# Kernel tuning notes

Hardware: AMD Instinct MI355X
Metric: run time of the kernel (lower is better)

## Reference

```python
import jax, jax.numpy as jnp
import numpy as np

B, T, S = 1, 8, 1024
HID, H = 1152, 16
D = HID // H  # 72
EPS = 1e-6


def rmsnorm(t, gamma):
    # t: [b,t,s,h,d], gamma: [h,d] per-head learnable scale (QKNorm)
    var = jnp.mean(jnp.square(t), axis=-1, keepdims=True)
    return t * jax.lax.rsqrt(var + EPS) * gamma


def setup_inputs() -> dict:
    key = jax.random.key(0)
    ks = jax.random.split(key, 8)
    sc = lambda fan_in: 1.0 / np.sqrt(fan_in)
    x = jax.random.normal(ks[0], (B, T, S, HID), dtype=jnp.float32)
    Wq = jax.random.normal(ks[1], (HID, HID), dtype=jnp.float32) * sc(HID)
    bq = jnp.zeros((HID,), dtype=jnp.float32)
    Wkv = jax.random.normal(ks[2], (HID, 2 * HID), dtype=jnp.float32) * sc(HID)
    bkv = jnp.zeros((2 * HID,), dtype=jnp.float32)
    q_gamma = jnp.ones((H, D), dtype=jnp.float32)
    k_gamma = jnp.ones((H, D), dtype=jnp.float32)
    Wo = jax.random.normal(ks[3], (HID, HID), dtype=jnp.float32) * sc(HID)
    return {"x": x, "Wq": Wq, "bq": bq, "Wkv": Wkv, "bkv": bkv,
            "q_gamma": q_gamma, "k_gamma": k_gamma, "Wo": Wo}


def reference(x, Wq, bq, Wkv, bkv, q_gamma, k_gamma, Wo):
    b, t, s, _ = x.shape
    q = (x @ Wq + bq).reshape(b, t, s, H, D)
    kv = x @ Wkv + bkv
    k, v = jnp.split(kv, 2, axis=-1)
    k = k.reshape(b, t, s, H, D)
    v = v.reshape(b, t, s, H, D)
    q = rmsnorm(q, q_gamma)
    k = rmsnorm(k, k_gamma)
    # NOTE: original applies no 1/sqrt(d) scaling (QKNorm replaces it)
    attn_weight = jnp.einsum('btqhd,btkhd->bthqk', q, k)
    attn = jax.nn.softmax(attn_weight, axis=-1)
    out = jnp.einsum('bthqk,btkhd->btqhd', attn, v).reshape(b, t, s, HID)
    return out @ Wo
```

## Files before the change

kernel.cpp:

```cpp
#include <hip/hip_runtime.h>


typedef __attribute__((ext_vector_type(4))) short s16x4;
typedef __attribute__((ext_vector_type(8))) short s16x8;
typedef __attribute__((ext_vector_type(4))) float f32x4;
typedef __attribute__((ext_vector_type(16))) float f32x16;

__device__ __forceinline__ unsigned short f2b(float x) {
  unsigned u = __float_as_uint(x);
  u += 0x7FFFu + ((u >> 16) & 1u);
  return (unsigned short)(u >> 16);
}
__device__ __forceinline__ float b2f(unsigned short u) {
  return __uint_as_float(((unsigned)u) << 16);
}
__device__ __forceinline__ void gld16(const void* g, void* l) {
  __builtin_amdgcn_global_load_lds(
      (const __attribute__((address_space(1))) void*)g,
      (__attribute__((address_space(3))) void*)l, 16, 0, 0);
}

__global__ __launch_bounds__(256) void cvt_bf16_kernel(const float* __restrict__ in,
                                                       unsigned short* __restrict__ out,
                                                       int n16) {
  int i = blockIdx.x * 256 + threadIdx.x;
  if (i >= n16) return;
  const float4* p = (const float4*)(in + (size_t)i * 16);
  float4 a = p[0], b = p[1], c = p[2], d = p[3];
  s16x8 r0, r1;
  r0[0] = (short)f2b(a.x); r0[1] = (short)f2b(a.y); r0[2] = (short)f2b(a.z); r0[3] = (short)f2b(a.w);
  r0[4] = (short)f2b(c.x); r0[5] = (short)f2b(c.y); r0[6] = (short)f2b(c.z); r0[7] = (short)f2b(c.w);
  r1[0] = (short)f2b(b.x); r1[1] = (short)f2b(b.y); r1[2] = (short)f2b(b.z); r1[3] = (short)f2b(b.w);
  r1[4] = (short)f2b(d.x); r1[5] = (short)f2b(d.y); r1[6] = (short)f2b(d.z); r1[7] = (short)f2b(d.w);
  *(s16x8*)(out + (size_t)i * 16) = r0;
  *(s16x8*)(out + (size_t)i * 16 + 8) = r1;
}

__global__ __launch_bounds__(256) void transpose_cvt_kernel(const float* __restrict__ W,
                                                            unsigned short* __restrict__ WT,
                                                            int K, int N) {
  __shared__ float tile[32][33];
  int n0 = blockIdx.x * 32, k0 = blockIdx.y * 32;
  int tx = threadIdx.x, ty = threadIdx.y;
#pragma unroll
  for (int i = 0; i < 4; i++)
    tile[ty + i * 8][tx] = W[(size_t)(k0 + ty + i * 8) * N + n0 + tx];
  __syncthreads();
  int stx = (tx & 19) | ((tx & 4) << 1) | ((tx & 8) >> 1);
#pragma unroll
  for (int i = 0; i < 4; i++)
    WT[(size_t)(n0 + ty + i * 8) * K + k0 + stx] = f2b(tile[tx][ty + i * 8]);
}

template <int MODE>
__global__ __launch_bounds__(256) void gemm_bt_kernel(const unsigned short* __restrict__ A,
                                                      const unsigned short* __restrict__ BT,
                                                      const float* __restrict__ biasq,
                                                      const float* __restrict__ biaskv,
                                                      int N, int gx,
                                                      float* __restrict__ outF,
                                                      unsigned short* __restrict__ qn,
                                                      unsigned short* __restrict__ kn,
                                                      unsigned short* __restrict__ vt) {
  constexpr int K = 1152;
  constexpr int NT = K / 32;
  __shared__ __align__(16) unsigned short As[3 * 4096];
  __shared__ __align__(16) unsigned short Bs[3 * 4096];
  int tid = threadIdx.x;
  int lane = tid & 63, wave = tid >> 6;
  int wr = (wave >> 1) * 64, wc = (wave & 1) * 64;
  int l31 = lane & 31, lh = lane >> 5;
  int bid = blockIdx.x;
  int xcd = bid & 7;
  int w = bid >> 3;
  int st = w / 24, inner = w - st * 24;
  int ibx = inner % 3, iby = inner / 3;
  int bx = st * 3 + ibx;
  int by = xcd * 8 + iby;
  int brow = by * 128, bcol = bx * 128;
  const unsigned short* AsrcP[2];
  const unsigned short* BsrcP[2];
  int dst0[2];
#pragma unroll
  for (int i = 0; i < 2; i++) {
    int c = tid + 256 * i;
    int row = c >> 2, j = c & 3;
    int ch = j ^ ((row >> 1) & 3);
    AsrcP[i] = A + (size_t)(brow + row) * K + ch * 8;
    BsrcP[i] = BT + (size_t)(bcol + row) * K + ch * 8;
    dst0[i] = (wave * 64 + 256 * i) * 8;
  }
#define STAGE(KT, BUF)                                          \
  {                                                             \
    int kb = (KT) * 32;                                         \
    gld16(AsrcP[0] + kb, &As[(BUF) * 4096 + dst0[0]]);          \
    gld16(BsrcP[0] + kb, &Bs[(BUF) * 4096 + dst0[0]]);          \
    gld16(AsrcP[1] + kb, &As[(BUF) * 4096 + dst0[1]]);          \
    gld16(BsrcP[1] + kb, &Bs[(BUF) * 4096 + dst0[1]]);          \
  }
  int fr = (l31 >> 1) & 3;
  int slotk[2] = {(lh ^ fr) * 8, ((2 + lh) ^ fr) * 8};
  STAGE(0, 0);
  STAGE(1, 1);
  f32x16 acc[2][2] = {};
  int cur = 0;
  for (int kt = 0; kt < NT; kt++) {
    if (kt < NT - 1)
      asm volatile("s_waitcnt vmcnt(4)\n\ts_barrier" ::: "memory");
    else
      asm volatile("s_waitcnt vmcnt(0)\n\ts_barrier" ::: "memory");
    if (kt + 2 < NT) {
      int nb = (cur == 0) ? 2 : cur - 1;
      STAGE(kt + 2, nb);
    }
    int ab = cur * 4096;
#pragma unroll
    for (int kk = 0; kk < 2; kk++) {
      int so = slotk[kk];
      s16x8 af[2], bf[2];
#pragma unroll
      for (int m = 0; m < 2; m++)
        af[m] = *(const s16x8*)&As[ab + (wr + m * 32 + l31) * 32 + so];
#pragma unroll
      for (int n = 0; n < 2; n++)
        bf[n] = *(const s16x8*)&Bs[ab + (wc + n * 32 + l31) * 32 + so];
      __builtin_amdgcn_s_setprio(1);
#pragma unroll
      for (int m = 0; m < 2; m++)
#pragma unroll
        for (int n = 0; n < 2; n++)
          acc[m][n] = __builtin_amdgcn_mfma_f32_32x32x16_bf16(af[m], bf[n], acc[m][n], 0, 0, 0);
      __builtin_amdgcn_s_setprio(0);
    }
    cur = (cur == 2) ? 0 : cur + 1;
  }
#undef STAGE
#pragma unroll
  for (int m = 0; m < 2; m++) {
#pragma unroll
    for (int n = 0; n < 2; n++) {
#pragma unroll
      for (int reg = 0; reg < 16; reg++) {
        int grow = brow + wr + m * 32 + (reg & 3) + 8 * (reg >> 2) + 4 * lh;
        int gcol = bcol + wc + n * 32 + l31;
        float v = acc[m][n][reg];
        if (MODE == 0) {
          outF[(size_t)grow * N + gcol] = v;
        } else {
          v += (gcol < 1152) ? biasq[gcol] : biaskv[gcol - 1152];
          int t = grow >> 10, s = grow & 1023;
          if (gcol < 2304) {
            int c = (gcol < 1152) ? gcol : gcol - 1152;
            int h = c / 72, d = c - h * 72;
            unsigned short* dst = (gcol < 1152) ? qn : kn;
            dst[((size_t)((t * 16 + h) * 1024 + s)) * 96 + d] = f2b(v);
          } else {
            int c = gcol - 2304;
            int h = c / 72, d = c - h * 72;
            vt[((size_t)((t * 16 + h) * 80 + d)) * 1024 + s] = f2b(v);
          }
        }
      }
    }
  }
}

__global__ __launch_bounds__(256) void rmsnorm2_kernel(unsigned short* __restrict__ qn,
                                                       unsigned short* __restrict__ kn,
                                                       const float* __restrict__ qg,
                                                       const float* __restrict__ kg) {
  int r = blockIdx.x * 4 + (threadIdx.x >> 6);
  int isK = r >= 131072;
  int g = isK ? r - 131072 : r;
  unsigned short* buf = isK ? kn : qn;
  const float* gamma = isK ? kg : qg;
  int h = (g >> 10) & 15;
  size_t base = (size_t)g * 96;
  int l = threadIdx.x & 63;
  float e0 = b2f(buf[base + l]);
  float e1 = 0.f;
  if (l < 8) e1 = b2f(buf[base + 64 + l]);
  float ss = e0 * e0 + e1 * e1;
#pragma unroll
  for (int m = 1; m < 64; m <<= 1) ss += __shfl_xor(ss, m);
  float sc = rsqrtf(ss * (1.0f / 72.0f) + 1e-6f);
  buf[base + l] = f2b(e0 * sc * gamma[h * 72 + l]);
  if (l < 32) {
    float v = 0.f;
    if (l < 8) v = e1 * sc * gamma[h * 72 + 64 + l];
    buf[base + 64 + l] = f2b(v);
  }
}

__global__ __launch_bounds__(256) void attn_kernel(const unsigned short* __restrict__ Qn,
                                                   const unsigned short* __restrict__ Kn,
                                                   const unsigned short* __restrict__ VtG,
                                                   unsigned short* __restrict__ att) {
  __shared__ unsigned short Kl[2][64][100];
  __shared__ unsigned short Vt[2][80][76];
  int tid = threadIdx.x;
  int lane = tid & 63, wave = tid >> 6;
  int l15 = lane & 15, lq = lane >> 4, kf = lq * 4;
  int bid = blockIdx.x;
  int orig = (bid & 7) * 256 + (bid >> 3);
  int qb = orig & 15, th = orig >> 4;
  int t = th >> 4, h = th & 15;
  const unsigned short* Q = Qn + (size_t)th * 1024 * 96;
  const unsigned short* Kp = Kn + (size_t)th * 1024 * 96;
  const unsigned short* Vg = VtG + (size_t)th * 80 * 1024;
  int qrow0 = qb * 64 + wave * 16;
  int krow[3], kco[3], vd[3], vco[3];
#pragma unroll
  for (int i = 0; i < 3; i++) {
    int c = tid + i * 256;
    krow[i] = c / 12;
    kco[i] = c - 12 * krow[i];
    int cc = tid + i * 256;
    vd[i] = cc >> 3;
    vco[i] = cc & 7;
  }
  bool v2 = tid < 128;
  s16x8 sk[3], sv[3];
  s16x8 qf[3];
#pragma unroll
  for (int c = 0; c < 3; c++) {
    const unsigned short* p = Q + (size_t)(qrow0 + l15) * 96 + c * 32 + kf;
    s16x4 lo = *(const s16x4*)p;
    s16x4 hi = *(const s16x4*)(p + 16);
    qf[c] = __builtin_shufflevector(lo, hi, 0, 1, 2, 3, 4, 5, 6, 7);
  }
  f32x4 o[5] = {};
  float m_r = -3.0e38f, l_r = 0.f;

#pragma unroll
  for (int i = 0; i < 3; i++)
    sk[i] = *(const s16x8*)(Kp + (size_t)krow[i] * 96 + kco[i] * 8);
#pragma unroll
  for (int i = 0; i < 2; i++)
    sv[i] = *(const s16x8*)(Vg + (size_t)vd[i] * 1024 + vco[i] * 8);
  if (v2) sv[2] = *(const s16x8*)(Vg + (size_t)vd[2] * 1024 + vco[2] * 8);
#pragma unroll
  for (int i = 0; i < 3; i++) *(s16x8*)&Kl[0][krow[i]][kco[i] * 8] = sk[i];
#pragma unroll
  for (int i = 0; i < 2; i++) *(s16x8*)&Vt[0][vd[i]][vco[i] * 8] = sv[i];
  if (v2) *(s16x8*)&Vt[0][vd[2]][vco[2] * 8] = sv[2];

  for (int tt = 0; tt < 16; tt++) {
    __syncthreads();
    int cur = tt & 1;
    if (tt < 15) {
      int kv1 = (tt + 1) * 64;
#pragma unroll
      for (int i = 0; i < 3; i++)
        sk[i] = *(const s16x8*)(Kp + (size_t)(kv1 + krow[i]) * 96 + kco[i] * 8);
#pragma unroll
      for (int i = 0; i < 2; i++)
        sv[i] = *(const s16x8*)(Vg + (size_t)vd[i] * 1024 + kv1 + vco[i] * 8);
      if (v2) sv[2] = *(const s16x8*)(Vg + (size_t)vd[2] * 1024 + kv1 + vco[2] * 8);
    }
    f32x4 st[4];
    __builtin_amdgcn_s_setprio(1);
#pragma unroll
    for (int n = 0; n < 4; n++) {
      f32x4 a = {};
#pragma unroll
      for (int c = 0; c < 3; c++) {
        s16x4 lo = *(const s16x4*)&Kl[cur][n * 16 + l15][c * 32 + kf];
        s16x4 hi = *(const s16x4*)&Kl[cur][n * 16 + l15][c * 32 + kf + 16];
        s16x8 kfr = __builtin_shufflevector(lo, hi, 0, 1, 2, 3, 4, 5, 6, 7);
        a = __builtin_amdgcn_mfma_f32_16x16x32_bf16(kfr, qf[c], a, 0, 0, 0);
      }
      st[n] = a;
    }
    __builtin_amdgcn_s_setprio(0);
    float tmax = st[0][0];
#pragma unroll
    for (int n = 0; n < 4; n++)
#pragma unroll
      for (int r = 0; r < 4; r++) tmax = fmaxf(tmax, st[n][r]);
    tmax = fmaxf(tmax, __shfl_xor(tmax, 16));
    tmax = fmaxf(tmax, __shfl_xor(tmax, 32));
    float mn = fmaxf(m_r, tmax);
    float scale = __expf(m_r - mn);
    m_r = mn;
    float sum = 0.f;
#pragma unroll
    for (int n = 0; n < 4; n++)
#pragma unroll
      for (int r = 0; r < 4; r++) {
        float p = __expf(st[n][r] - mn);
        st[n][r] = p;
        sum += p;
      }
    sum += __shfl_xor(sum, 16);
    sum += __shfl_xor(sum, 32);
    l_r = l_r * scale + sum;
#pragma unroll
    for (int r = 0; r < 4; r++) {
      float scq = __shfl(scale, 4 * lq + r);
#pragma unroll
      for (int v = 0; v < 5; v++) o[v][r] *= scq;
    }
    __builtin_amdgcn_s_setprio(1);
#pragma unroll
    for (int b = 0; b < 2; b++) {
      s16x8 pf;
#pragma unroll
      for (int j = 0; j < 8; j++) pf[j] = (short)f2b(st[2 * b + (j >> 2)][j & 3]);
#pragma unroll
      for (int v = 0; v < 5; v++) {
        s16x4 vlo = *(const s16x4*)&Vt[cur][v * 16 + l15][b * 32 + kf];
        s16x4 vhi = *(const s16x4*)&Vt[cur][v * 16 + l15][b * 32 + kf + 16];
        s16x8 vf = __builtin_shufflevector(vlo, vhi, 0, 1, 2, 3, 4, 5, 6, 7);
        o[v] = __builtin_amdgcn_mfma_f32_16x16x32_bf16(pf, vf, o[v], 0, 0, 0);
      }
    }
    __builtin_amdgcn_s_setprio(0);
    if (tt < 15) {
      int nxt = cur ^ 1;
#pragma unroll
      for (int i = 0; i < 3; i++) *(s16x8*)&Kl[nxt][krow[i]][kco[i] * 8] = sk[i];
#pragma unroll
      for (int i = 0; i < 2; i++) *(s16x8*)&Vt[nxt][vd[i]][vco[i] * 8] = sv[i];
      if (v2) *(s16x8*)&Vt[nxt][vd[2]][vco[2] * 8] = sv[2];
    }
  }
#pragma unroll
  for (int r = 0; r < 4; r++) {
    float inv = 1.0f / __shfl(l_r, 4 * lq + r);
    int qrow = qrow0 + 4 * lq + r;
    size_t rowbase = (size_t)(t * 1024 + qrow) * 1152;
#pragma unroll
    for (int v = 0; v < 5; v++) {
      int d = v * 16 + l15;
      if (d < 72) {
        int col = h * 72 + d;
        int scol = (col & ~12) | ((col & 4) << 1) | ((col & 8) >> 1);
        att[rowbase + scol] = f2b(o[v][r] * inv);
      }
    }
  }
}

extern "C" void kernel_launch(void* const* d_in, const int* in_sizes, int n_in,
                              void* d_out, int out_size, void* d_ws, size_t ws_size,
                              hipStream_t stream) {
  const float* x   = (const float*)d_in[0];
  const float* Wq  = (const float*)d_in[1];
  const float* bq  = (const float*)d_in[2];
  const float* Wkv = (const float*)d_in[3];
  const float* bkv = (const float*)d_in[4];
  const float* qg  = (const float*)d_in[5];
  const float* kg  = (const float*)d_in[6];
  const float* Wo  = (const float*)d_in[7];
  float* out = (float*)d_out;

  char* w = (char*)d_ws;
  unsigned short* xb   = (unsigned short*)w; w += (size_t)8192 * 1152 * 2;
  unsigned short* WqT  = (unsigned short*)w; w += (size_t)1152 * 1152 * 2;
  unsigned short* WkvT = (unsigned short*)w; w += (size_t)2304 * 1152 * 2;
  unsigned short* WoT  = (unsigned short*)w; w += (size_t)1152 * 1152 * 2;
  unsigned short* qn   = (unsigned short*)w; w += (size_t)128 * 1024 * 96 * 2;
  unsigned short* kn   = (unsigned short*)w; w += (size_t)128 * 1024 * 96 * 2;
  unsigned short* vt   = (unsigned short*)w; w += (size_t)128 * 80 * 1024 * 2;
  unsigned short* att  = (unsigned short*)w; w += (size_t)8192 * 1152 * 2;

  cvt_bf16_kernel<<<2304, 256, 0, stream>>>(x, xb, 9437184 / 16);
  transpose_cvt_kernel<<<dim3(36, 36), dim3(32, 8), 0, stream>>>(Wq, WqT, 1152, 1152);
  transpose_cvt_kernel<<<dim3(72, 36), dim3(32, 8), 0, stream>>>(Wkv, WkvT, 1152, 2304);
  transpose_cvt_kernel<<<dim3(36, 36), dim3(32, 8), 0, stream>>>(Wo, WoT, 1152, 1152);

  gemm_bt_kernel<3><<<1728, 256, 0, stream>>>(xb, WqT, bq, bkv, 3456, 27, nullptr, qn, kn, vt);
  rmsnorm2_kernel<<<65536, 256, 0, stream>>>(qn, kn, qg, kg);

  attn_kernel<<<2048, 256, 0, stream>>>(qn, kn, vt, att);

  gemm_bt_kernel<0><<<576, 256, 0, stream>>>(att, WoT, nullptr, nullptr, 1152, 9, out, nullptr, nullptr, nullptr);
}
```

Before: 313.3 us.

## Use 256x256 tiles with 8 waves for the fused QKV projection GEMM

Replaces the 128x128, 4-wave QKV GEMM with a dedicated 512-thread kernel that computes 256x256 output tiles. It loads the A and B stages in two halves interleaved with MFMA phases and uses XOR-swizzled LDS addressing. Each block grows its per-block data reuse and uses fewer blocks, which should cut global and LDS traffic per flop. The N dimension (3456) does not divide evenly into 256-wide tiles, so a zeroed pad region after WkvT absorbs the out-of-range B reads and the epilogue skips those columns. The tradeoffs are higher register and LDS pressure, fewer blocks (448) for the CUs to share, and a tail tile that spends compute on padding.

```diff
diff --git a/kernel.cpp b/kernel.cpp
--- a/kernel.cpp
+++ b/kernel.cpp
@@ -52,16 +52,133 @@
     WT[(size_t)(n0 + ty + i * 8) * K + k0 + stx] = f2b(tile[tx][ty + i * 8]);
 }
 
-template <int MODE>
-__global__ __launch_bounds__(256) void gemm_bt_kernel(const unsigned short* __restrict__ A,
-                                                      const unsigned short* __restrict__ BT,
-                                                      const float* __restrict__ biasq,
-                                                      const float* __restrict__ biaskv,
-                                                      int N, int gx,
-                                                      float* __restrict__ outF,
-                                                      unsigned short* __restrict__ qn,
-                                                      unsigned short* __restrict__ kn,
-                                                      unsigned short* __restrict__ vt) {
+__global__ __launch_bounds__(512, 2) void gemm_qkv_kernel(const unsigned short* __restrict__ A,
+                                                          const unsigned short* __restrict__ BT,
+                                                          const float* __restrict__ biasq,
+                                                          const float* __restrict__ biaskv,
+                                                          unsigned short* __restrict__ qn,
+                                                          unsigned short* __restrict__ kn,
+                                                          unsigned short* __restrict__ vt) {
+  constexpr int K = 1152;
+  constexpr int NT = 36;
+  __shared__ __align__(16) unsigned short As[3][8192];
+  __shared__ __align__(16) unsigned short Bs[3][8192];
+  int tid = threadIdx.x;
+  int lane = tid & 63, wave = tid >> 6;
+  int wm = wave >> 2, wn = wave & 3;
+  int wr = wm * 128, wc = wn * 64;
+  int l31 = lane & 31, lh = lane >> 5;
+  int bid = blockIdx.x;
+  int xcd = bid & 7, w = bid >> 3;
+  int iby = w / 14, ibx = w - iby * 14;
+  int brow = (xcd * 4 + iby) * 256, bcol = ibx * 256;
+  int d1 = wave * 128 + lane, d2 = d1 + 64;
+  int r1 = d1 >> 2, j1 = d1 & 3;
+  int r2 = d2 >> 2, j2 = d2 & 3;
+  const unsigned short* A1 = A + (size_t)(brow + r1) * K + (j1 ^ ((r1 >> 1) & 3)) * 8;
+  const unsigned short* A2 = A + (size_t)(brow + r2) * K + (j2 ^ ((r2 >> 1) & 3)) * 8;
+  const unsigned short* B1 = BT + (size_t)(bcol + r1) * K + (j1 ^ ((r1 >> 1) & 3)) * 8;
+  const unsigned short* B2 = BT + (size_t)(bcol + r2) * K + (j2 ^ ((r2 >> 1) & 3)) * 8;
+  int dstL = wave * 1024, dstH = wave * 1024 + 512;
+#define STAGE_A(KT, BUF) { gld16(A1 + (KT) * 32, &As[BUF][dstL]); gld16(A2 + (KT) * 32, &As[BUF][dstH]); }
+#define STAGE_B(KT, BUF) { gld16(B1 + (KT) * 32, &Bs[BUF][dstL]); gld16(B2 + (KT) * 32, &Bs[BUF][dstH]); }
+  int rA[4], fA[4], rB[2], fB[2];
+#pragma unroll
+  for (int m = 0; m < 4; m++) { rA[m] = wr + m * 32 + l31; fA[m] = (rA[m] >> 1) & 3; }
+#pragma unroll
+  for (int n = 0; n < 2; n++) { rB[n] = wc + n * 32 + l31; fB[n] = (rB[n] >> 1) & 3; }
+  STAGE_A(0, 0); STAGE_B(0, 0);
+  STAGE_A(1, 1); STAGE_B(1, 1);
+  asm volatile("s_waitcnt vmcnt(4)" ::: "memory");
+  __builtin_amdgcn_s_barrier();
+  f32x16 acc[4][2] = {};
+  int cur = 0;
+  for (int t = 0; t < NT; t++) {
+    int nxt = cur + 2; if (nxt >= 3) nxt -= 3;
+    s16x8 a0[2][2], b0[2][2];
+#pragma unroll
+    for (int m = 0; m < 2; m++)
+#pragma unroll
+      for (int ks = 0; ks < 2; ks++)
+        a0[m][ks] = *(const s16x8*)&As[cur][rA[m] * 32 + ((2 * ks + lh) ^ fA[m]) * 8];
+#pragma unroll
+    for (int n = 0; n < 2; n++)
+#pragma unroll
+      for (int ks = 0; ks < 2; ks++)
+        b0[n][ks] = *(const s16x8*)&Bs[cur][rB[n] * 32 + ((2 * ks + lh) ^ fB[n]) * 8];
+    if (t + 2 < NT) STAGE_A(t + 2, nxt);
+    __builtin_amdgcn_s_barrier();
+    asm volatile("s_waitcnt lgkmcnt(0)" ::: "memory");
+    __builtin_amdgcn_sched_barrier(0);
+    __builtin_amdgcn_s_setprio(1);
+#pragma unroll
+    for (int m = 0; m < 2; m++)
+#pragma unroll
+      for (int n = 0; n < 2; n++)
+#pragma unroll
+        for (int ks = 0; ks < 2; ks++)
+          acc[m][n] = __builtin_amdgcn_mfma_f32_32x32x16_bf16(a0[m][ks], b0[n][ks], acc[m][n], 0, 0, 0);
+    __builtin_amdgcn_s_setprio(0);
+    s16x8 a1[2][2];
+#pragma unroll
+    for (int m = 0; m < 2; m++)
+#pragma unroll
+      for (int ks = 0; ks < 2; ks++)
+        a1[m][ks] = *(const s16x8*)&As[cur][rA[m + 2] * 32 + ((2 * ks + lh) ^ fA[m + 2]) * 8];
+    if (t + 2 < NT) STAGE_B(t + 2, nxt);
+    __builtin_amdgcn_s_barrier();
+    asm volatile("s_waitcnt lgkmcnt(0)" ::: "memory");
+    __builtin_amdgcn_sched_barrier(0);
+    __builtin_amdgcn_s_setprio(1);
+#pragma unroll
+    for (int m = 0; m < 2; m++)
+#pragma unroll
+      for (int n = 0; n < 2; n++)
+#pragma unroll
+        for (int ks = 0; ks < 2; ks++)
+          acc[m + 2][n] = __builtin_amdgcn_mfma_f32_32x32x16_bf16(a1[m][ks], b0[n][ks], acc[m + 2][n], 0, 0, 0);
+    __builtin_amdgcn_s_setprio(0);
+    if (t < NT - 1) {
+      if (t < NT - 2)
+        asm volatile("s_waitcnt vmcnt(4)" ::: "memory");
+      else
+        asm volatile("s_waitcnt vmcnt(0)" ::: "memory");
+      __builtin_amdgcn_s_barrier();
+    }
+    cur = cur + 1; if (cur >= 3) cur = 0;
+  }
+#undef STAGE_A
+#undef STAGE_B
+#pragma unroll
+  for (int m = 0; m < 4; m++) {
+#pragma unroll
+    for (int n = 0; n < 2; n++) {
+      int gcol = bcol + wc + n * 32 + l31;
+      if (gcol >= 3456) continue;
+      float bias = (gcol < 1152) ? biasq[gcol] : biaskv[gcol - 1152];
+      int c = (gcol < 1152) ? gcol : (gcol < 2304 ? gcol - 1152 : gcol - 2304);
+      int h = c / 72, d = c - h * 72;
+      int rowbase = brow + wr + m * 32 + 4 * lh;
+#pragma unroll
+      for (int reg = 0; reg < 16; reg++) {
+        int grow = rowbase + (reg & 3) + 8 * (reg >> 2);
+        float v = acc[m][n][reg] + bias;
+        int t = grow >> 10, s = grow & 1023;
+        if (gcol < 2304) {
+          unsigned short* dst = (gcol < 1152) ? qn : kn;
+          dst[((size_t)((t * 16 + h) * 1024 + s)) * 96 + d] = f2b(v);
+        } else {
+          vt[((size_t)((t * 16 + h) * 80 + d)) * 1024 + s] = f2b(v);
+        }
+      }
+    }
+  }
+}
+
+__global__ __launch_bounds__(256) void gemm_out_kernel(const unsigned short* __restrict__ A,
+                                                       const unsigned short* __restrict__ BT,
+                                                       int N, int gx,
+                                                       float* __restrict__ outF) {
   constexpr int K = 1152;
   constexpr int NT = K / 32;
   __shared__ __align__(16) unsigned short As[3 * 4096];
@@ -143,23 +260,7 @@
       for (int reg = 0; reg < 16; reg++) {
         int grow = brow + wr + m * 32 + (reg & 3) + 8 * (reg >> 2) + 4 * lh;
         int gcol = bcol + wc + n * 32 + l31;
-        float v = acc[m][n][reg];
-        if (MODE == 0) {
-          outF[(size_t)grow * N + gcol] = v;
-        } else {
-          v += (gcol < 1152) ? biasq[gcol] : biaskv[gcol - 1152];
-          int t = grow >> 10, s = grow & 1023;
-          if (gcol < 2304) {
-            int c = (gcol < 1152) ? gcol : gcol - 1152;
-            int h = c / 72, d = c - h * 72;
-            unsigned short* dst = (gcol < 1152) ? qn : kn;
-            dst[((size_t)((t * 16 + h) * 1024 + s)) * 96 + d] = f2b(v);
-          } else {
-            int c = gcol - 2304;
-            int h = c / 72, d = c - h * 72;
-            vt[((size_t)((t * 16 + h) * 80 + d)) * 1024 + s] = f2b(v);
-          }
-        }
+        outF[(size_t)grow * N + gcol] = acc[m][n][reg];
       }
     }
   }
@@ -359,21 +460,23 @@
   unsigned short* xb   = (unsigned short*)w; w += (size_t)8192 * 1152 * 2;
   unsigned short* WqT  = (unsigned short*)w; w += (size_t)1152 * 1152 * 2;
   unsigned short* WkvT = (unsigned short*)w; w += (size_t)2304 * 1152 * 2;
+  unsigned short* Wpad = (unsigned short*)w; w += (size_t)128 * 1152 * 2;
   unsigned short* WoT  = (unsigned short*)w; w += (size_t)1152 * 1152 * 2;
   unsigned short* qn   = (unsigned short*)w; w += (size_t)128 * 1024 * 96 * 2;
   unsigned short* kn   = (unsigned short*)w; w += (size_t)128 * 1024 * 96 * 2;
   unsigned short* vt   = (unsigned short*)w; w += (size_t)128 * 80 * 1024 * 2;
   unsigned short* att  = (unsigned short*)w; w += (size_t)8192 * 1152 * 2;
 
+  hipMemsetAsync(Wpad, 0, (size_t)128 * 1152 * 2, stream);
   cvt_bf16_kernel<<<2304, 256, 0, stream>>>(x, xb, 9437184 / 16);
   transpose_cvt_kernel<<<dim3(36, 36), dim3(32, 8), 0, stream>>>(Wq, WqT, 1152, 1152);
   transpose_cvt_kernel<<<dim3(72, 36), dim3(32, 8), 0, stream>>>(Wkv, WkvT, 1152, 2304);
   transpose_cvt_kernel<<<dim3(36, 36), dim3(32, 8), 0, stream>>>(Wo, WoT, 1152, 1152);
 
-  gemm_bt_kernel<3><<<1728, 256, 0, stream>>>(xb, WqT, bq, bkv, 3456, 27, nullptr, qn, kn, vt);
+  gemm_qkv_kernel<<<448, 512, 0, stream>>>(xb, WqT, bq, bkv, qn, kn, vt);
   rmsnorm2_kernel<<<65536, 256, 0, stream>>>(qn, kn, qg, kg);
 
   attn_kernel<<<2048, 256, 0, stream>>>(qn, kn, vt, att);
 
-  gemm_bt_kernel<0><<<576, 256, 0, stream>>>(att, WoT, nullptr, nullptr, 1152, 9, out, nullptr, nullptr, nullptr);
-}
+  gemm_out_kernel<<<576, 256, 0, stream>>>(att, WoT, 1152, 9, out);
+}
```

Result: slower. 322.0 us (+2.8%).
